# Performance work log

Measured on AMD Instinct MI355X. Metric: run time of the kernel, lower is better.

The kernel has to match this reference:

```python
import jax, jax.numpy as jnp
import numpy as np

HEADS = 16
EMBED = 1024
HEAD_DIM = EMBED // HEADS


def setup_inputs() -> dict:
    key = jax.random.key(0)
    ks = jax.random.split(key, 10)
    B, SQ, SKV = 2, 2048, 2048
    s = 1.0 / np.sqrt(HEAD_DIM)
    sd = 1.0 / np.sqrt(EMBED)
    return {
        "queries": jax.random.normal(ks[0], (B, SQ, EMBED), jnp.float32),
        "values": jax.random.normal(ks[1], (B, SKV, EMBED), jnp.float32),
        "heads": HEADS,
        "Wv": jax.random.normal(ks[2], (HEAD_DIM, HEAD_DIM), jnp.float32) * s,
        "bv": jax.random.normal(ks[3], (HEAD_DIM,), jnp.float32) * 0.02,
        "Wk": jax.random.normal(ks[4], (HEAD_DIM, HEAD_DIM), jnp.float32) * s,
        "bk": jax.random.normal(ks[5], (HEAD_DIM,), jnp.float32) * 0.02,
        "Wq": jax.random.normal(ks[6], (HEAD_DIM, HEAD_DIM), jnp.float32) * s,
        "bq": jax.random.normal(ks[7], (HEAD_DIM,), jnp.float32) * 0.02,
        "Wd": jax.random.normal(ks[8], (EMBED, EMBED), jnp.float32) * sd,
        "bd": jax.random.normal(ks[9], (EMBED,), jnp.float32) * 0.02,
    }


def reference(queries, values, heads, Wv, bv, Wk, bk, Wq, bq, Wd, bd):
    n, sq, e = queries.shape
    skv = values.shape[1]
    d = e // heads
    # reshape to per-head layout [b, s, h, d]
    q_in = queries.reshape(n, sq, heads, d)
    v_in = values.reshape(n, skv, heads, d)
    # shared per-head linear projections (torch Linear: x @ W.T + b)
    v = jnp.einsum("bshd,ed->bshe", v_in, Wv) + bv
    # quirk preserved: keys computed from the ALREADY-PROJECTED values
    k = jnp.einsum("bshd,ed->bshe", v, Wk) + bk
    q = jnp.einsum("bshd,ed->bshe", q_in, Wq) + bq
    # full O(n^2) score matrix [b, h, sq, skv] (as in source)
    scores = jnp.einsum("bqhd,bkhd->bhqk", q, k) / jnp.sqrt(jnp.asarray(d, q.dtype))
    attn = jax.nn.softmax(scores, axis=-1)
    out = jnp.einsum("bhqk,bkhd->bqhd", attn, v).reshape(n, sq, e)
    return out @ Wd.T + bd
```

## Files before the change

### kernel.cpp

```cpp
#include <hip/hip_runtime.h>
#include <hip/hip_bf16.h>
#include <hip/hip_fp16.h>
#include <math.h>

typedef _Float16 f16;
typedef _Float16 f16x8 __attribute__((ext_vector_type(8)));
typedef _Float16 f16x4 __attribute__((ext_vector_type(4)));
typedef _Float16 f16x2 __attribute__((ext_vector_type(2)));
typedef unsigned short u16x8v __attribute__((ext_vector_type(8)));
typedef float f32x4 __attribute__((ext_vector_type(4)));

namespace {
constexpr int B = 2;
constexpr int H = 16;
constexpr int S = 2048;
constexpr int D = 64;
constexpr int E = 1024;
constexpr int LP = 72;
constexpr float QSCALE = 0.125f * 1.4426950408889634f;
}

__global__ void make_wkv(const float* __restrict__ Wk, const float* __restrict__ Wv,
                         const float* __restrict__ bv, const float* __restrict__ bk,
                         float* __restrict__ Wkv, float* __restrict__ bkv) {
  const int g = blockIdx.x * 256 + threadIdx.x;
  const int i = g >> 6, j = g & 63;
  float s = 0.f;
#pragma unroll 16
  for (int d = 0; d < 64; ++d) s = fmaf(Wk[i * 64 + d], Wv[d * 64 + j], s);
  Wkv[g] = s;
  if (g < 64) {
    float bb = bk[g];
#pragma unroll 16
    for (int d = 0; d < 64; ++d) bb = fmaf(Wk[g * 64 + d], bv[d], bb);
    bkv[g] = bb;
  }
}

__global__ __launch_bounds__(256) void cvt_wd(const float* __restrict__ W, f16* __restrict__ out) {
  const int i = blockIdx.x * 256 + threadIdx.x;
  const float4 f = ((const float4*)W)[i];
  f16x4 o;
  o.x = (f16)f.x; o.y = (f16)f.y; o.z = (f16)f.z; o.w = (f16)f.w;
  *(f16x4*)(out + 4 * (size_t)i) = o;
}

__global__ __launch_bounds__(256) void proj_mfma(const float* __restrict__ x,
                                                 const float* __restrict__ W,
                                                 const float* __restrict__ bias,
                                                 f16* __restrict__ out, float scale) {
  const int t = threadIdx.x, lane = t & 63, w = t >> 6;
  const int l15 = lane & 15, quad = lane >> 4;
  const int m0 = (blockIdx.x * 4 + w) * 64;

  f16x8 wf[4][2], af[4][2];
#pragma unroll
  for (int nt = 0; nt < 4; ++nt)
#pragma unroll
    for (int kc = 0; kc < 2; ++kc) {
      const float* g = W + (size_t)(nt * 16 + l15) * 64 + kc * 32 + quad * 8;
      const float4 a = *(const float4*)g, b2 = *(const float4*)(g + 4);
      f16x8 v;
      v[0]=(f16)a.x; v[1]=(f16)a.y; v[2]=(f16)a.z; v[3]=(f16)a.w;
      v[4]=(f16)b2.x; v[5]=(f16)b2.y; v[6]=(f16)b2.z; v[7]=(f16)b2.w;
      wf[nt][kc] = v;
    }
#pragma unroll
  for (int mt = 0; mt < 4; ++mt)
#pragma unroll
    for (int kc = 0; kc < 2; ++kc) {
      const float* g = x + (size_t)(m0 + mt * 16 + l15) * 64 + kc * 32 + quad * 8;
      const float4 a = *(const float4*)g, b2 = *(const float4*)(g + 4);
      f16x8 v;
      v[0]=(f16)a.x; v[1]=(f16)a.y; v[2]=(f16)a.z; v[3]=(f16)a.w;
      v[4]=(f16)b2.x; v[5]=(f16)b2.y; v[6]=(f16)b2.z; v[7]=(f16)b2.w;
      af[mt][kc] = v;
    }

  f32x4 acc[4][4];
#pragma unroll
  for (int mt = 0; mt < 4; ++mt)
#pragma unroll
    for (int nt = 0; nt < 4; ++nt) acc[mt][nt] = (f32x4){0.f, 0.f, 0.f, 0.f};
#pragma unroll
  for (int kc = 0; kc < 2; ++kc)
#pragma unroll
    for (int nt = 0; nt < 4; ++nt)
#pragma unroll
      for (int mt = 0; mt < 4; ++mt)
        acc[mt][nt] = __builtin_amdgcn_mfma_f32_16x16x32_f16(af[mt][kc], wf[nt][kc], acc[mt][nt], 0, 0, 0);

  float bl[4];
#pragma unroll
  for (int nt = 0; nt < 4; ++nt) bl[nt] = bias[nt * 16 + l15];

#pragma unroll
  for (int mt = 0; mt < 4; ++mt)
#pragma unroll
    for (int r = 0; r < 4; ++r) {
      const int g = m0 + mt * 16 + quad * 4 + r;
      const int h = g & 15, bs = g >> 4;
      const int b = bs >> 11, s = bs & 2047;
      f16* o = out + ((size_t)(b * H + h) * S + s) * 64;
#pragma unroll
      for (int nt = 0; nt < 4; ++nt)
        o[nt * 16 + l15] = (f16)((acc[mt][nt][r] + bl[nt]) * scale);
    }
}

__global__ __launch_bounds__(256) void attn_mfma(const f16* __restrict__ qp,
                                                 const f16* __restrict__ kp,
                                                 const f16* __restrict__ vp,
                                                 f16* __restrict__ ao) {
  __shared__ f16 ks[64 * LP];
  __shared__ f16 vt[64 * LP];
  __shared__ f16 ps[4 * 32 * LP];
  const int t = threadIdx.x, lane = t & 63, w = t >> 6;
  const int l15 = lane & 15, quad = lane >> 4;
  const int bh = blockIdx.x;
  const int q0 = blockIdx.y * 128;
  const f16* qbase = qp + ((size_t)bh * S + q0 + w * 32) * D;
  const f16* kbase = kp + (size_t)bh * S * D;
  const f16* vbase = vp + (size_t)bh * S * D;
  f16* pw = ps + w * 32 * LP;

  f16x8 qf[2][2];
#pragma unroll
  for (int mt = 0; mt < 2; ++mt)
#pragma unroll
    for (int kc = 0; kc < 2; ++kc)
      qf[mt][kc] = *(const f16x8*)(qbase + (size_t)(mt * 16 + l15) * D + kc * 32 + quad * 8);

  f16x8 vb4;
#pragma unroll
  for (int j = 0; j < 8; ++j) vb4[j] = (l15 == 0) ? (f16)1.0f : (f16)0.0f;

  f32x4 O[2][5];
#pragma unroll
  for (int mt = 0; mt < 2; ++mt)
#pragma unroll
    for (int nt = 0; nt < 5; ++nt) O[mt][nt] = (f32x4){0.f, 0.f, 0.f, 0.f};

  for (int kt = 0; kt < S / 64; ++kt) {
    __syncthreads();
    {
      const int r = t >> 2, c0 = (t & 3) * 16;
      const f16* g = kbase + ((size_t)kt * 64 + r) * D + c0;
      *(f16x8*)&ks[r * LP + c0] = *(const f16x8*)g;
      *(f16x8*)&ks[r * LP + c0 + 8] = *(const f16x8*)(g + 8);
    }
    {
      const int d0 = (t >> 5) * 8, pc0 = (t & 31) * 2;
      const int kva = (pc0 & 3) * 16 + (pc0 >> 2);
      const u16x8v a = *(const u16x8v*)(vbase + ((size_t)kt * 64 + kva) * D + d0);
      const u16x8v b2 = *(const u16x8v*)(vbase + ((size_t)kt * 64 + kva + 16) * D + d0);
#pragma unroll
      for (int j = 0; j < 8; ++j) {
        const unsigned pk = (unsigned)a[j] | ((unsigned)b2[j] << 16);
        *(unsigned*)&vt[(d0 + j) * LP + pc0] = pk;
      }
    }
    __syncthreads();

    f32x4 sc[2][4];
#pragma unroll
    for (int mt = 0; mt < 2; ++mt)
#pragma unroll
      for (int nt = 0; nt < 4; ++nt) sc[mt][nt] = (f32x4){0.f, 0.f, 0.f, 0.f};
#pragma unroll
    for (int kc = 0; kc < 2; ++kc)
#pragma unroll
      for (int nt = 0; nt < 4; ++nt) {
        const f16x8 bf = *(const f16x8*)&ks[(nt * 16 + l15) * LP + kc * 32 + quad * 8];
#pragma unroll
        for (int mt = 0; mt < 2; ++mt)
          sc[mt][nt] = __builtin_amdgcn_mfma_f32_16x16x32_f16(qf[mt][kc], bf, sc[mt][nt], 0, 0, 0);
      }

#pragma unroll
    for (int mt = 0; mt < 2; ++mt)
#pragma unroll
      for (int r = 0; r < 4; ++r) {
        const float p0 = __builtin_amdgcn_exp2f(sc[mt][0][r]);
        const float p1 = __builtin_amdgcn_exp2f(sc[mt][1][r]);
        const float p2 = __builtin_amdgcn_exp2f(sc[mt][2][r]);
        const float p3 = __builtin_amdgcn_exp2f(sc[mt][3][r]);
        union { f16x4 v4; f16x2 h[2]; } u;
        u.h[0] = __builtin_bit_cast(f16x2, __builtin_amdgcn_cvt_pkrtz(p0, p1));
        u.h[1] = __builtin_bit_cast(f16x2, __builtin_amdgcn_cvt_pkrtz(p2, p3));
        *(f16x4*)&pw[(mt * 16 + quad * 4 + r) * LP + l15 * 4] = u.v4;
      }
    __asm__ volatile("s_waitcnt lgkmcnt(0)" ::: "memory");

    f16x8 pa[2][2];
#pragma unroll
    for (int mt = 0; mt < 2; ++mt)
#pragma unroll
      for (int kc = 0; kc < 2; ++kc)
        pa[mt][kc] = *(const f16x8*)&pw[(mt * 16 + l15) * LP + kc * 32 + quad * 8];
#pragma unroll
    for (int kc = 0; kc < 2; ++kc) {
#pragma unroll
      for (int nt = 0; nt < 4; ++nt) {
        const f16x8 vbf = *(const f16x8*)&vt[(nt * 16 + l15) * LP + kc * 32 + quad * 8];
#pragma unroll
        for (int mt = 0; mt < 2; ++mt)
          O[mt][nt] = __builtin_amdgcn_mfma_f32_16x16x32_f16(pa[mt][kc], vbf, O[mt][nt], 0, 0, 0);
      }
#pragma unroll
      for (int mt = 0; mt < 2; ++mt)
        O[mt][4] = __builtin_amdgcn_mfma_f32_16x16x32_f16(pa[mt][kc], vb4, O[mt][4], 0, 0, 0);
    }
  }

  const int b = bh >> 4, h = bh & 15;
#pragma unroll
  for (int mt = 0; mt < 2; ++mt)
#pragma unroll
    for (int r = 0; r < 4; ++r) {
      const float l = __shfl(O[mt][4][r], quad << 4, 64);
      const float inv = 1.f / l;
      const int row = q0 + w * 32 + mt * 16 + quad * 4 + r;
      f16* o = ao + ((size_t)b * S + row) * E + h * D;
#pragma unroll
      for (int nt = 0; nt < 4; ++nt)
        o[nt * 16 + l15] = (f16)(O[mt][nt][r] * inv);
    }
}

__global__ __launch_bounds__(256) void dense_mfma(const f16* __restrict__ A,
                                                  const f16* __restrict__ Wd16,
                                                  const float* __restrict__ bd,
                                                  float* __restrict__ out) {
  __shared__ f16 as[128 * LP];
  __shared__ f16 bs[128 * LP];
  const int t = threadIdx.x;
  const int lane = t & 63;
  const int w = t >> 6;
  const int l15 = lane & 15;
  const int quad = lane >> 4;
  const int m0 = blockIdx.x * 128;
  const int n0 = blockIdx.y * 128;
  const int wm = (w >> 1) * 64, wn = (w & 1) * 64;

  f32x4 acc[4][4];
#pragma unroll
  for (int mt = 0; mt < 4; ++mt)
#pragma unroll
    for (int nt = 0; nt < 4; ++nt) acc[mt][nt] = (f32x4){0.f, 0.f, 0.f, 0.f};

  for (int kt = 0; kt < E / 64; ++kt) {
    __syncthreads();
    {
      const int r = t >> 1, c0 = (t & 1) * 32;
      const f16* ga = A + (size_t)(m0 + r) * E + kt * 64 + c0;
      const f16* gb = Wd16 + (size_t)(n0 + r) * E + kt * 64 + c0;
#pragma unroll
      for (int c = 0; c < 4; ++c) {
        *(f16x8*)&as[r * LP + c0 + 8 * c] = *(const f16x8*)(ga + 8 * c);
        *(f16x8*)&bs[r * LP + c0 + 8 * c] = *(const f16x8*)(gb + 8 * c);
      }
    }
    __syncthreads();
    f16x8 af[4][2];
#pragma unroll
    for (int mt = 0; mt < 4; ++mt)
#pragma unroll
      for (int kc = 0; kc < 2; ++kc)
        af[mt][kc] = *(const f16x8*)&as[(wm + mt * 16 + l15) * LP + kc * 32 + quad * 8];
#pragma unroll
    for (int kc = 0; kc < 2; ++kc)
#pragma unroll
      for (int nt = 0; nt < 4; ++nt) {
        const f16x8 bf = *(const f16x8*)&bs[(wn + nt * 16 + l15) * LP + kc * 32 + quad * 8];
#pragma unroll
        for (int mt = 0; mt < 4; ++mt)
          acc[mt][nt] = __builtin_amdgcn_mfma_f32_16x16x32_f16(af[mt][kc], bf, acc[mt][nt], 0, 0, 0);
      }
  }
#pragma unroll
  for (int nt = 0; nt < 4; ++nt) {
    const int col = n0 + wn + nt * 16 + l15;
    const float bdv = bd[col];
#pragma unroll
    for (int mt = 0; mt < 4; ++mt)
#pragma unroll
      for (int r = 0; r < 4; ++r)
        out[(size_t)(m0 + wm + mt * 16 + quad * 4 + r) * E + col] = acc[mt][nt][r] + bdv;
  }
}

extern "C" void kernel_launch(void* const* d_in, const int* in_sizes, int n_in,
                              void* d_out, int out_size, void* d_ws, size_t ws_size,
                              hipStream_t stream) {
  const float* queries = (const float*)d_in[0];
  const float* values  = (const float*)d_in[1];
  const float* Wv = (const float*)d_in[3];
  const float* bv = (const float*)d_in[4];
  const float* Wk = (const float*)d_in[5];
  const float* bk = (const float*)d_in[6];
  const float* Wq = (const float*)d_in[7];
  const float* bq = (const float*)d_in[8];
  const float* Wd = (const float*)d_in[9];
  const float* bd = (const float*)d_in[10];
  float* out = (float*)d_out;

  char* ws = (char*)d_ws;
  f16* qp    = (f16*)(ws);
  f16* kp    = (f16*)(ws + 8u * 1024 * 1024);
  f16* vp    = (f16*)(ws + 16u * 1024 * 1024);
  f16* ao    = (f16*)(ws + 24u * 1024 * 1024);
  f16* wd16  = (f16*)(ws + 32u * 1024 * 1024);
  float* wkv = (float*)(ws + 34u * 1024 * 1024);
  float* bkv = (float*)(ws + 34u * 1024 * 1024 + 16384);
  (void)ws_size; (void)in_sizes; (void)n_in; (void)out_size;

  make_wkv<<<16, 256, 0, stream>>>(Wk, Wv, bv, bk, wkv, bkv);
  cvt_wd<<<E * E / 1024, 256, 0, stream>>>(Wd, wd16);
  proj_mfma<<<256, 256, 0, stream>>>(queries, Wq, bq, qp, QSCALE);
  proj_mfma<<<256, 256, 0, stream>>>(values, Wv, bv, vp, 1.0f);
  proj_mfma<<<256, 256, 0, stream>>>(values, wkv, bkv, kp, 1.0f);
  attn_mfma<<<dim3(B * H, S / 128), 256, 0, stream>>>(qp, kp, vp, ao);
  dense_mfma<<<dim3(B * S / 128, E / 128), 256, 0, stream>>>(ao, wd16, bd, out);
}
```

Baseline: 198.6 us.

## Fuse V/K projections, pre-transpose V, load attention and dense operands from global

```diff
diff --git a/kernel.cpp b/kernel.cpp
--- a/kernel.cpp
+++ b/kernel.cpp
@@ -108,12 +108,116 @@
     }
 }
 
-__global__ __launch_bounds__(256) void attn_mfma(const f16* __restrict__ qp,
-                                                 const f16* __restrict__ kp,
-                                                 const f16* __restrict__ vp,
-                                                 f16* __restrict__ ao) {
-  __shared__ f16 ks[64 * LP];
-  __shared__ f16 vt[64 * LP];
+__global__ __launch_bounds__(256) void proj_vk_mfma(const float* __restrict__ x,
+                                                    const float* __restrict__ Wv,
+                                                    const float* __restrict__ bv,
+                                                    const float* __restrict__ Wkv,
+                                                    const float* __restrict__ bkv,
+                                                    f16* __restrict__ vout,
+                                                    f16* __restrict__ kout) {
+  const int t = threadIdx.x, lane = t & 63, w = t >> 6;
+  const int l15 = lane & 15, quad = lane >> 4;
+  const int m0 = (blockIdx.x * 4 + w) * 32;
+
+  f16x8 wfv[4][2], wfk[4][2], af[2][2];
+#pragma unroll
+  for (int nt = 0; nt < 4; ++nt)
+#pragma unroll
+    for (int kc = 0; kc < 2; ++kc) {
+      const size_t off = (size_t)(nt * 16 + l15) * 64 + kc * 32 + quad * 8;
+      {
+        const float4 a = *(const float4*)(Wv + off), b2 = *(const float4*)(Wv + off + 4);
+        f16x8 v;
+        v[0]=(f16)a.x; v[1]=(f16)a.y; v[2]=(f16)a.z; v[3]=(f16)a.w;
+        v[4]=(f16)b2.x; v[5]=(f16)b2.y; v[6]=(f16)b2.z; v[7]=(f16)b2.w;
+        wfv[nt][kc] = v;
+      }
+      {
+        const float4 a = *(const float4*)(Wkv + off), b2 = *(const float4*)(Wkv + off + 4);
+        f16x8 v;
+        v[0]=(f16)a.x; v[1]=(f16)a.y; v[2]=(f16)a.z; v[3]=(f16)a.w;
+        v[4]=(f16)b2.x; v[5]=(f16)b2.y; v[6]=(f16)b2.z; v[7]=(f16)b2.w;
+        wfk[nt][kc] = v;
+      }
+    }
+#pragma unroll
+  for (int mt = 0; mt < 2; ++mt)
+#pragma unroll
+    for (int kc = 0; kc < 2; ++kc) {
+      const float* g = x + (size_t)(m0 + mt * 16 + l15) * 64 + kc * 32 + quad * 8;
+      const float4 a = *(const float4*)g, b2 = *(const float4*)(g + 4);
+      f16x8 v;
+      v[0]=(f16)a.x; v[1]=(f16)a.y; v[2]=(f16)a.z; v[3]=(f16)a.w;
+      v[4]=(f16)b2.x; v[5]=(f16)b2.y; v[6]=(f16)b2.z; v[7]=(f16)b2.w;
+      af[mt][kc] = v;
+    }
+
+  f32x4 accv[2][4], acck[2][4];
+#pragma unroll
+  for (int mt = 0; mt < 2; ++mt)
+#pragma unroll
+    for (int nt = 0; nt < 4; ++nt) {
+      accv[mt][nt] = (f32x4){0.f, 0.f, 0.f, 0.f};
+      acck[mt][nt] = (f32x4){0.f, 0.f, 0.f, 0.f};
+    }
+#pragma unroll
+  for (int kc = 0; kc < 2; ++kc)
+#pragma unroll
+    for (int nt = 0; nt < 4; ++nt)
+#pragma unroll
+      for (int mt = 0; mt < 2; ++mt) {
+        accv[mt][nt] = __builtin_amdgcn_mfma_f32_16x16x32_f16(af[mt][kc], wfv[nt][kc], accv[mt][nt], 0, 0, 0);
+        acck[mt][nt] = __builtin_amdgcn_mfma_f32_16x16x32_f16(af[mt][kc], wfk[nt][kc], acck[mt][nt], 0, 0, 0);
+      }
+
+  float blv[4], blk[4];
+#pragma unroll
+  for (int nt = 0; nt < 4; ++nt) { blv[nt] = bv[nt * 16 + l15]; blk[nt] = bkv[nt * 16 + l15]; }
+
+#pragma unroll
+  for (int mt = 0; mt < 2; ++mt)
+#pragma unroll
+    for (int r = 0; r < 4; ++r) {
+      const int g = m0 + mt * 16 + quad * 4 + r;
+      const int h = g & 15, bs = g >> 4;
+      const int b = bs >> 11, s = bs & 2047;
+      const size_t o = ((size_t)(b * H + h) * S + s) * 64;
+#pragma unroll
+      for (int nt = 0; nt < 4; ++nt) {
+        vout[o + nt * 16 + l15] = (f16)(accv[mt][nt][r] + blv[nt]);
+        kout[o + nt * 16 + l15] = (f16)(acck[mt][nt][r] + blk[nt]);
+      }
+    }
+}
+
+__global__ __launch_bounds__(256) void transpose_v(const f16* __restrict__ vp,
+                                                   f16* __restrict__ vtg) {
+  __shared__ f16 lvt[64 * LP];
+  const int t = threadIdx.x;
+  const int bh = blockIdx.x, kt = blockIdx.y;
+  const f16* vb = vp + ((size_t)bh * S + kt * 64) * D;
+  {
+    const int d0 = (t >> 5) * 8, pc0 = (t & 31) * 2;
+    const int kva = (pc0 & 3) * 16 + (pc0 >> 2);
+    const u16x8v a = *(const u16x8v*)(vb + (size_t)kva * D + d0);
+    const u16x8v b2 = *(const u16x8v*)(vb + (size_t)(kva + 16) * D + d0);
+#pragma unroll
+    for (int j = 0; j < 8; ++j) {
+      const unsigned pk = (unsigned)a[j] | ((unsigned)b2[j] << 16);
+      *(unsigned*)&lvt[(d0 + j) * LP + pc0] = pk;
+    }
+  }
+  __syncthreads();
+  const int d = t >> 2, pc = (t & 3) * 16;
+  f16* o = vtg + ((size_t)bh * D + d) * S + kt * 64 + pc;
+  *(f16x8*)o = *(const f16x8*)&lvt[d * LP + pc];
+  *(f16x8*)(o + 8) = *(const f16x8*)&lvt[d * LP + pc + 8];
+}
+
+__global__ __launch_bounds__(256, 2) void attn_mfma(const f16* __restrict__ qp,
+                                                    const f16* __restrict__ kp,
+                                                    const f16* __restrict__ vtg,
+                                                    f16* __restrict__ ao) {
   __shared__ f16 ps[4 * 32 * LP];
   const int t = threadIdx.x, lane = t & 63, w = t >> 6;
   const int l15 = lane & 15, quad = lane >> 4;
@@ -121,7 +225,7 @@
   const int q0 = blockIdx.y * 128;
   const f16* qbase = qp + ((size_t)bh * S + q0 + w * 32) * D;
   const f16* kbase = kp + (size_t)bh * S * D;
-  const f16* vbase = vp + (size_t)bh * S * D;
+  const f16* vbase = vtg + (size_t)bh * D * S;
   f16* pw = ps + w * 32 * LP;
 
   f16x8 qf[2][2];
@@ -141,26 +245,16 @@
 #pragma unroll
     for (int nt = 0; nt < 5; ++nt) O[mt][nt] = (f32x4){0.f, 0.f, 0.f, 0.f};
 
+  f16x8 kf[2][2][4];
+#pragma unroll
+  for (int kc = 0; kc < 2; ++kc)
+#pragma unroll
+    for (int nt = 0; nt < 4; ++nt)
+      kf[0][kc][nt] = *(const f16x8*)(kbase + (size_t)(nt * 16 + l15) * D + kc * 32 + quad * 8);
+
+#pragma unroll 2
   for (int kt = 0; kt < S / 64; ++kt) {
-    __syncthreads();
-    {
-      const int r = t >> 2, c0 = (t & 3) * 16;
-      const f16* g = kbase + ((size_t)kt * 64 + r) * D + c0;
-      *(f16x8*)&ks[r * LP + c0] = *(const f16x8*)g;
-      *(f16x8*)&ks[r * LP + c0 + 8] = *(const f16x8*)(g + 8);
-    }
-    {
-      const int d0 = (t >> 5) * 8, pc0 = (t & 31) * 2;
-      const int kva = (pc0 & 3) * 16 + (pc0 >> 2);
-      const u16x8v a = *(const u16x8v*)(vbase + ((size_t)kt * 64 + kva) * D + d0);
-      const u16x8v b2 = *(const u16x8v*)(vbase + ((size_t)kt * 64 + kva + 16) * D + d0);
-#pragma unroll
-      for (int j = 0; j < 8; ++j) {
-        const unsigned pk = (unsigned)a[j] | ((unsigned)b2[j] << 16);
-        *(unsigned*)&vt[(d0 + j) * LP + pc0] = pk;
-      }
-    }
-    __syncthreads();
+    const int cur = kt & 1, nxt = cur ^ 1;
 
     f32x4 sc[2][4];
 #pragma unroll
@@ -170,12 +264,24 @@
 #pragma unroll
     for (int kc = 0; kc < 2; ++kc)
 #pragma unroll
-      for (int nt = 0; nt < 4; ++nt) {
-        const f16x8 bf = *(const f16x8*)&ks[(nt * 16 + l15) * LP + kc * 32 + quad * 8];
+      for (int nt = 0; nt < 4; ++nt)
 #pragma unroll
         for (int mt = 0; mt < 2; ++mt)
-          sc[mt][nt] = __builtin_amdgcn_mfma_f32_16x16x32_f16(qf[mt][kc], bf, sc[mt][nt], 0, 0, 0);
-      }
+          sc[mt][nt] = __builtin_amdgcn_mfma_f32_16x16x32_f16(qf[mt][kc], kf[cur][kc][nt], sc[mt][nt], 0, 0, 0);
+
+    const int ktn = (kt + 1) & (S / 64 - 1);
+#pragma unroll
+    for (int kc = 0; kc < 2; ++kc)
+#pragma unroll
+      for (int nt = 0; nt < 4; ++nt)
+        kf[nxt][kc][nt] = *(const f16x8*)(kbase + ((size_t)ktn * 64 + nt * 16 + l15) * D + kc * 32 + quad * 8);
+
+    f16x8 vf[2][4];
+#pragma unroll
+    for (int kc = 0; kc < 2; ++kc)
+#pragma unroll
+      for (int nt = 0; nt < 4; ++nt)
+        vf[kc][nt] = *(const f16x8*)(vbase + (size_t)(nt * 16 + l15) * S + kt * 64 + kc * 32 + quad * 8);
 
 #pragma unroll
     for (int mt = 0; mt < 2; ++mt)
@@ -198,15 +304,14 @@
 #pragma unroll
       for (int kc = 0; kc < 2; ++kc)
         pa[mt][kc] = *(const f16x8*)&pw[(mt * 16 + l15) * LP + kc * 32 + quad * 8];
-#pragma unroll
-    for (int kc = 0; kc < 2; ++kc) {
-#pragma unroll
-      for (int nt = 0; nt < 4; ++nt) {
-        const f16x8 vbf = *(const f16x8*)&vt[(nt * 16 + l15) * LP + kc * 32 + quad * 8];
+
+#pragma unroll
+    for (int kc = 0; kc < 2; ++kc) {
+#pragma unroll
+      for (int nt = 0; nt < 4; ++nt)
 #pragma unroll
         for (int mt = 0; mt < 2; ++mt)
-          O[mt][nt] = __builtin_amdgcn_mfma_f32_16x16x32_f16(pa[mt][kc], vbf, O[mt][nt], 0, 0, 0);
-      }
+          O[mt][nt] = __builtin_amdgcn_mfma_f32_16x16x32_f16(pa[mt][kc], vf[kc][nt], O[mt][nt], 0, 0, 0);
 #pragma unroll
       for (int mt = 0; mt < 2; ++mt)
         O[mt][4] = __builtin_amdgcn_mfma_f32_16x16x32_f16(pa[mt][kc], vb4, O[mt][4], 0, 0, 0);
@@ -232,15 +337,9 @@
                                                   const f16* __restrict__ Wd16,
                                                   const float* __restrict__ bd,
                                                   float* __restrict__ out) {
-  __shared__ f16 as[128 * LP];
-  __shared__ f16 bs[128 * LP];
-  const int t = threadIdx.x;
-  const int lane = t & 63;
-  const int w = t >> 6;
-  const int l15 = lane & 15;
-  const int quad = lane >> 4;
-  const int m0 = blockIdx.x * 128;
-  const int n0 = blockIdx.y * 128;
+  const int t = threadIdx.x, lane = t & 63, w = t >> 6;
+  const int l15 = lane & 15, quad = lane >> 4;
+  const int m0 = blockIdx.x * 128, n0 = blockIdx.y * 128;
   const int wm = (w >> 1) * 64, wn = (w & 1) * 64;
 
   f32x4 acc[4][4];
@@ -249,34 +348,23 @@
 #pragma unroll
     for (int nt = 0; nt < 4; ++nt) acc[mt][nt] = (f32x4){0.f, 0.f, 0.f, 0.f};
 
+#pragma unroll
   for (int kt = 0; kt < E / 64; ++kt) {
-    __syncthreads();
-    {
-      const int r = t >> 1, c0 = (t & 1) * 32;
-      const f16* ga = A + (size_t)(m0 + r) * E + kt * 64 + c0;
-      const f16* gb = Wd16 + (size_t)(n0 + r) * E + kt * 64 + c0;
-#pragma unroll
-      for (int c = 0; c < 4; ++c) {
-        *(f16x8*)&as[r * LP + c0 + 8 * c] = *(const f16x8*)(ga + 8 * c);
-        *(f16x8*)&bs[r * LP + c0 + 8 * c] = *(const f16x8*)(gb + 8 * c);
-      }
-    }
-    __syncthreads();
-    f16x8 af[4][2];
-#pragma unroll
-    for (int mt = 0; mt < 4; ++mt)
-#pragma unroll
-      for (int kc = 0; kc < 2; ++kc)
-        af[mt][kc] = *(const f16x8*)&as[(wm + mt * 16 + l15) * LP + kc * 32 + quad * 8];
-#pragma unroll
-    for (int kc = 0; kc < 2; ++kc)
-#pragma unroll
-      for (int nt = 0; nt < 4; ++nt) {
-        const f16x8 bf = *(const f16x8*)&bs[(wn + nt * 16 + l15) * LP + kc * 32 + quad * 8];
+#pragma unroll
+    for (int kc = 0; kc < 2; ++kc) {
+      f16x8 af[4], bf[4];
+#pragma unroll
+      for (int mt = 0; mt < 4; ++mt)
+        af[mt] = *(const f16x8*)(A + (size_t)(m0 + wm + mt * 16 + l15) * E + kt * 64 + kc * 32 + quad * 8);
+#pragma unroll
+      for (int nt = 0; nt < 4; ++nt)
+        bf[nt] = *(const f16x8*)(Wd16 + (size_t)(n0 + wn + nt * 16 + l15) * E + kt * 64 + kc * 32 + quad * 8);
+#pragma unroll
+      for (int nt = 0; nt < 4; ++nt)
 #pragma unroll
         for (int mt = 0; mt < 4; ++mt)
-          acc[mt][nt] = __builtin_amdgcn_mfma_f32_16x16x32_f16(af[mt][kc], bf, acc[mt][nt], 0, 0, 0);
-      }
+          acc[mt][nt] = __builtin_amdgcn_mfma_f32_16x16x32_f16(af[mt], bf[nt], acc[mt][nt], 0, 0, 0);
+    }
   }
 #pragma unroll
   for (int nt = 0; nt < 4; ++nt) {
@@ -313,13 +401,14 @@
   f16* wd16  = (f16*)(ws + 32u * 1024 * 1024);
   float* wkv = (float*)(ws + 34u * 1024 * 1024);
   float* bkv = (float*)(ws + 34u * 1024 * 1024 + 16384);
+  f16* vtg   = (f16*)(ws + 36u * 1024 * 1024);
   (void)ws_size; (void)in_sizes; (void)n_in; (void)out_size;
 
   make_wkv<<<16, 256, 0, stream>>>(Wk, Wv, bv, bk, wkv, bkv);
   cvt_wd<<<E * E / 1024, 256, 0, stream>>>(Wd, wd16);
   proj_mfma<<<256, 256, 0, stream>>>(queries, Wq, bq, qp, QSCALE);
-  proj_mfma<<<256, 256, 0, stream>>>(values, Wv, bv, vp, 1.0f);
-  proj_mfma<<<256, 256, 0, stream>>>(values, wkv, bkv, kp, 1.0f);
-  attn_mfma<<<dim3(B * H, S / 128), 256, 0, stream>>>(qp, kp, vp, ao);
+  proj_vk_mfma<<<512, 256, 0, stream>>>(values, Wv, bv, wkv, bkv, vp, kp);
+  transpose_v<<<dim3(B * H, S / 64), 256, 0, stream>>>(vp, vtg);
+  attn_mfma<<<dim3(B * H, S / 128), 256, 0, stream>>>(qp, kp, vtg, ao);
   dense_mfma<<<dim3(B * S / 128, E / 128), 256, 0, stream>>>(ao, wd16, bd, out);
 }
```

New measurement: 274.6 us. 1.38x slower.

## Fuse V/K projections, use transposed-V attention, and convert Wd inside the dense GEMM

Applied to the files above, without the earlier changes.

```diff
diff --git a/kernel.cpp b/kernel.cpp
--- a/kernel.cpp
+++ b/kernel.cpp
@@ -7,8 +7,10 @@
 typedef _Float16 f16x8 __attribute__((ext_vector_type(8)));
 typedef _Float16 f16x4 __attribute__((ext_vector_type(4)));
 typedef _Float16 f16x2 __attribute__((ext_vector_type(2)));
-typedef unsigned short u16x8v __attribute__((ext_vector_type(8)));
 typedef float f32x4 __attribute__((ext_vector_type(4)));
+
+#define MFMA16(a, b, c) __builtin_amdgcn_mfma_f32_16x16x16f16((a), (b), (c), 0, 0, 0)
+#define MFMA32(a, b, c) __builtin_amdgcn_mfma_f32_16x16x32_f16((a), (b), (c), 0, 0, 0)
 
 namespace {
 constexpr int B = 2;
@@ -20,40 +22,22 @@
 constexpr float QSCALE = 0.125f * 1.4426950408889634f;
 }
 
-__global__ void make_wkv(const float* __restrict__ Wk, const float* __restrict__ Wv,
-                         const float* __restrict__ bv, const float* __restrict__ bk,
-                         float* __restrict__ Wkv, float* __restrict__ bkv) {
-  const int g = blockIdx.x * 256 + threadIdx.x;
-  const int i = g >> 6, j = g & 63;
-  float s = 0.f;
-#pragma unroll 16
-  for (int d = 0; d < 64; ++d) s = fmaf(Wk[i * 64 + d], Wv[d * 64 + j], s);
-  Wkv[g] = s;
-  if (g < 64) {
-    float bb = bk[g];
-#pragma unroll 16
-    for (int d = 0; d < 64; ++d) bb = fmaf(Wk[g * 64 + d], bv[d], bb);
-    bkv[g] = bb;
-  }
-}
-
-__global__ __launch_bounds__(256) void cvt_wd(const float* __restrict__ W, f16* __restrict__ out) {
-  const int i = blockIdx.x * 256 + threadIdx.x;
-  const float4 f = ((const float4*)W)[i];
-  f16x4 o;
-  o.x = (f16)f.x; o.y = (f16)f.y; o.z = (f16)f.z; o.w = (f16)f.w;
-  *(f16x4*)(out + 4 * (size_t)i) = o;
-}
-
-__global__ __launch_bounds__(256) void proj_mfma(const float* __restrict__ x,
-                                                 const float* __restrict__ W,
-                                                 const float* __restrict__ bias,
-                                                 f16* __restrict__ out, float scale) {
+__device__ __forceinline__ f16x4 cvt4(float a, float b, float c, float d) {
+  union { f16x4 v4; f16x2 h[2]; } u;
+  u.h[0] = __builtin_bit_cast(f16x2, __builtin_amdgcn_cvt_pkrtz(a, b));
+  u.h[1] = __builtin_bit_cast(f16x2, __builtin_amdgcn_cvt_pkrtz(c, d));
+  return u.v4;
+}
+
+__global__ __launch_bounds__(256) void proj_q(const float* __restrict__ x,
+                                              const float* __restrict__ W,
+                                              const float* __restrict__ bias,
+                                              f16* __restrict__ out) {
   const int t = threadIdx.x, lane = t & 63, w = t >> 6;
   const int l15 = lane & 15, quad = lane >> 4;
-  const int m0 = (blockIdx.x * 4 + w) * 64;
-
-  f16x8 wf[4][2], af[4][2];
+  const int m0 = (blockIdx.x * 4 + w) * 32;
+
+  f16x8 wf[4][2], af[2][2];
 #pragma unroll
   for (int nt = 0; nt < 4; ++nt)
 #pragma unroll
@@ -66,7 +50,7 @@
       wf[nt][kc] = v;
     }
 #pragma unroll
-  for (int mt = 0; mt < 4; ++mt)
+  for (int mt = 0; mt < 2; ++mt)
 #pragma unroll
     for (int kc = 0; kc < 2; ++kc) {
       const float* g = x + (size_t)(m0 + mt * 16 + l15) * 64 + kc * 32 + quad * 8;
@@ -77,9 +61,9 @@
       af[mt][kc] = v;
     }
 
-  f32x4 acc[4][4];
-#pragma unroll
-  for (int mt = 0; mt < 4; ++mt)
+  f32x4 acc[2][4];
+#pragma unroll
+  for (int mt = 0; mt < 2; ++mt)
 #pragma unroll
     for (int nt = 0; nt < 4; ++nt) acc[mt][nt] = (f32x4){0.f, 0.f, 0.f, 0.f};
 #pragma unroll
@@ -87,15 +71,15 @@
 #pragma unroll
     for (int nt = 0; nt < 4; ++nt)
 #pragma unroll
-      for (int mt = 0; mt < 4; ++mt)
-        acc[mt][nt] = __builtin_amdgcn_mfma_f32_16x16x32_f16(af[mt][kc], wf[nt][kc], acc[mt][nt], 0, 0, 0);
+      for (int mt = 0; mt < 2; ++mt)
+        acc[mt][nt] = MFMA32(af[mt][kc], wf[nt][kc], acc[mt][nt]);
 
   float bl[4];
 #pragma unroll
   for (int nt = 0; nt < 4; ++nt) bl[nt] = bias[nt * 16 + l15];
 
 #pragma unroll
-  for (int mt = 0; mt < 4; ++mt)
+  for (int mt = 0; mt < 2; ++mt)
 #pragma unroll
     for (int r = 0; r < 4; ++r) {
       const int g = m0 + mt * 16 + quad * 4 + r;
@@ -104,42 +88,132 @@
       f16* o = out + ((size_t)(b * H + h) * S + s) * 64;
 #pragma unroll
       for (int nt = 0; nt < 4; ++nt)
-        o[nt * 16 + l15] = (f16)((acc[mt][nt][r] + bl[nt]) * scale);
-    }
+        o[nt * 16 + l15] = (f16)((acc[mt][nt][r] + bl[nt]) * QSCALE);
+    }
+}
+
+__global__ __launch_bounds__(256) void proj_vk(const float* __restrict__ x,
+                                               const float* __restrict__ Wv,
+                                               const float* __restrict__ bv,
+                                               const float* __restrict__ Wk,
+                                               const float* __restrict__ bk,
+                                               f16* __restrict__ vtg,
+                                               f16* __restrict__ kp) {
+  const int t = threadIdx.x, lane = t & 63, w = t >> 6;
+  const int l15 = lane & 15, quad = lane >> 4;
+  const int bh = blockIdx.x;
+  const int b = bh >> 4, h = bh & 15;
+  const int s0 = blockIdx.y * 128 + w * 32;
+
+  f16x4 xb[2][4];
+#pragma unroll
+  for (int nt = 0; nt < 2; ++nt)
+#pragma unroll
+    for (int kc = 0; kc < 4; ++kc) {
+      const float4 f = *(const float4*)(x + ((size_t)(b * S + s0 + nt * 16 + l15)) * E + h * 64 + kc * 16 + quad * 4);
+      f16x4 v; v[0]=(f16)f.x; v[1]=(f16)f.y; v[2]=(f16)f.z; v[3]=(f16)f.w;
+      xb[nt][kc] = v;
+    }
+
+  f32x4 av[4][2];
+#pragma unroll
+  for (int mt = 0; mt < 4; ++mt)
+#pragma unroll
+    for (int nt = 0; nt < 2; ++nt) av[mt][nt] = (f32x4){0.f, 0.f, 0.f, 0.f};
+#pragma unroll
+  for (int kc = 0; kc < 4; ++kc) {
+    f16x4 wvf[4];
+#pragma unroll
+    for (int mt = 0; mt < 4; ++mt) {
+      const float4 f = *(const float4*)(Wv + (size_t)(mt * 16 + l15) * 64 + kc * 16 + quad * 4);
+      f16x4 v; v[0]=(f16)f.x; v[1]=(f16)f.y; v[2]=(f16)f.z; v[3]=(f16)f.w;
+      wvf[mt] = v;
+    }
+#pragma unroll
+    for (int mt = 0; mt < 4; ++mt)
+#pragma unroll
+      for (int nt = 0; nt < 2; ++nt)
+        av[mt][nt] = MFMA16(wvf[mt], xb[nt][kc], av[mt][nt]);
+  }
+
+  f16x4 vB[4][2];
+#pragma unroll
+  for (int mt = 0; mt < 4; ++mt) {
+    const float4 bb = *(const float4*)(bv + mt * 16 + quad * 4);
+#pragma unroll
+    for (int nt = 0; nt < 2; ++nt) {
+      const float v0 = av[mt][nt][0] + bb.x;
+      const float v1 = av[mt][nt][1] + bb.y;
+      const float v2 = av[mt][nt][2] + bb.z;
+      const float v3 = av[mt][nt][3] + bb.w;
+      const f16x4 pk = cvt4(v0, v1, v2, v3);
+      vB[mt][nt] = pk;
+      const int sc = s0 + nt * 16 + l15;
+      f16* vo = vtg + ((size_t)bh * 64 + mt * 16 + quad * 4) * S + sc;
+      vo[0 * S] = pk[0]; vo[1 * S] = pk[1]; vo[2 * S] = pk[2]; vo[3 * S] = pk[3];
+    }
+  }
+
+  f32x4 ak[4][2];
+#pragma unroll
+  for (int mt = 0; mt < 4; ++mt)
+#pragma unroll
+    for (int nt = 0; nt < 2; ++nt) ak[mt][nt] = (f32x4){0.f, 0.f, 0.f, 0.f};
+#pragma unroll
+  for (int ch = 0; ch < 4; ++ch) {
+    f16x4 wkf[4];
+#pragma unroll
+    for (int mt = 0; mt < 4; ++mt) {
+      const float4 f = *(const float4*)(Wk + (size_t)(mt * 16 + l15) * 64 + ch * 16 + quad * 4);
+      f16x4 v; v[0]=(f16)f.x; v[1]=(f16)f.y; v[2]=(f16)f.z; v[3]=(f16)f.w;
+      wkf[mt] = v;
+    }
+#pragma unroll
+    for (int mt = 0; mt < 4; ++mt)
+#pragma unroll
+      for (int nt = 0; nt < 2; ++nt)
+        ak[mt][nt] = MFMA16(wkf[mt], vB[ch][nt], ak[mt][nt]);
+  }
+#pragma unroll
+  for (int mt = 0; mt < 4; ++mt) {
+    const float4 bb = *(const float4*)(bk + mt * 16 + quad * 4);
+#pragma unroll
+    for (int nt = 0; nt < 2; ++nt) {
+      const int sc = s0 + nt * 16 + l15;
+      const f16x4 pk = cvt4(ak[mt][nt][0] + bb.x, ak[mt][nt][1] + bb.y,
+                            ak[mt][nt][2] + bb.z, ak[mt][nt][3] + bb.w);
+      *(f16x4*)(kp + ((size_t)bh * S + sc) * 64 + mt * 16 + quad * 4) = pk;
+    }
+  }
 }
 
 __global__ __launch_bounds__(256) void attn_mfma(const f16* __restrict__ qp,
                                                  const f16* __restrict__ kp,
-                                                 const f16* __restrict__ vp,
+                                                 const f16* __restrict__ vtg,
                                                  f16* __restrict__ ao) {
   __shared__ f16 ks[64 * LP];
   __shared__ f16 vt[64 * LP];
-  __shared__ f16 ps[4 * 32 * LP];
   const int t = threadIdx.x, lane = t & 63, w = t >> 6;
   const int l15 = lane & 15, quad = lane >> 4;
   const int bh = blockIdx.x;
   const int q0 = blockIdx.y * 128;
   const f16* qbase = qp + ((size_t)bh * S + q0 + w * 32) * D;
   const f16* kbase = kp + (size_t)bh * S * D;
-  const f16* vbase = vp + (size_t)bh * S * D;
-  f16* pw = ps + w * 32 * LP;
-
-  f16x8 qf[2][2];
-#pragma unroll
-  for (int mt = 0; mt < 2; ++mt)
-#pragma unroll
-    for (int kc = 0; kc < 2; ++kc)
-      qf[mt][kc] = *(const f16x8*)(qbase + (size_t)(mt * 16 + l15) * D + kc * 32 + quad * 8);
-
-  f16x8 vb4;
-#pragma unroll
-  for (int j = 0; j < 8; ++j) vb4[j] = (l15 == 0) ? (f16)1.0f : (f16)0.0f;
-
-  f32x4 O[2][5];
-#pragma unroll
-  for (int mt = 0; mt < 2; ++mt)
-#pragma unroll
-    for (int nt = 0; nt < 5; ++nt) O[mt][nt] = (f32x4){0.f, 0.f, 0.f, 0.f};
+  const f16* vbase = vtg + (size_t)bh * 64 * S;
+
+  f16x4 qf[2][4];
+#pragma unroll
+  for (int nt = 0; nt < 2; ++nt)
+#pragma unroll
+    for (int kc = 0; kc < 4; ++kc)
+      qf[nt][kc] = *(const f16x4*)(qbase + (size_t)(nt * 16 + l15) * D + kc * 16 + quad * 4);
+
+  f32x4 Ot[4][2];
+#pragma unroll
+  for (int dt = 0; dt < 4; ++dt)
+#pragma unroll
+    for (int nt = 0; nt < 2; ++nt) Ot[dt][nt] = (f32x4){0.f, 0.f, 0.f, 0.f};
+  float lsum[2] = {0.f, 0.f};
 
   for (int kt = 0; kt < S / 64; ++kt) {
     __syncthreads();
@@ -150,102 +224,93 @@
       *(f16x8*)&ks[r * LP + c0 + 8] = *(const f16x8*)(g + 8);
     }
     {
-      const int d0 = (t >> 5) * 8, pc0 = (t & 31) * 2;
-      const int kva = (pc0 & 3) * 16 + (pc0 >> 2);
-      const u16x8v a = *(const u16x8v*)(vbase + ((size_t)kt * 64 + kva) * D + d0);
-      const u16x8v b2 = *(const u16x8v*)(vbase + ((size_t)kt * 64 + kva + 16) * D + d0);
-#pragma unroll
-      for (int j = 0; j < 8; ++j) {
-        const unsigned pk = (unsigned)a[j] | ((unsigned)b2[j] << 16);
-        *(unsigned*)&vt[(d0 + j) * LP + pc0] = pk;
+      const int r = t >> 2, c0 = (t & 3) * 16;
+      const f16* g = vbase + (size_t)r * S + kt * 64 + c0;
+      *(f16x8*)&vt[r * LP + c0] = *(const f16x8*)g;
+      *(f16x8*)&vt[r * LP + c0 + 8] = *(const f16x8*)(g + 8);
+    }
+    __syncthreads();
+
+    f32x4 sc[4][2];
+#pragma unroll
+    for (int mt = 0; mt < 4; ++mt)
+#pragma unroll
+      for (int nt = 0; nt < 2; ++nt) sc[mt][nt] = (f32x4){0.f, 0.f, 0.f, 0.f};
+#pragma unroll
+    for (int kc = 0; kc < 4; ++kc) {
+      f16x4 ka[4];
+#pragma unroll
+      for (int mt = 0; mt < 4; ++mt)
+        ka[mt] = *(const f16x4*)&ks[(mt * 16 + l15) * LP + kc * 16 + quad * 4];
+#pragma unroll
+      for (int mt = 0; mt < 4; ++mt)
+#pragma unroll
+        for (int nt = 0; nt < 2; ++nt)
+          sc[mt][nt] = MFMA16(ka[mt], qf[nt][kc], sc[mt][nt]);
+    }
+
+    f16x4 pb[4][2];
+#pragma unroll
+    for (int mt = 0; mt < 4; ++mt)
+#pragma unroll
+      for (int nt = 0; nt < 2; ++nt) {
+        const float p0 = __builtin_amdgcn_exp2f(sc[mt][nt][0]);
+        const float p1 = __builtin_amdgcn_exp2f(sc[mt][nt][1]);
+        const float p2 = __builtin_amdgcn_exp2f(sc[mt][nt][2]);
+        const float p3 = __builtin_amdgcn_exp2f(sc[mt][nt][3]);
+        lsum[nt] += (p0 + p1) + (p2 + p3);
+        pb[mt][nt] = cvt4(p0, p1, p2, p3);
       }
-    }
-    __syncthreads();
-
-    f32x4 sc[2][4];
-#pragma unroll
-    for (int mt = 0; mt < 2; ++mt)
-#pragma unroll
-      for (int nt = 0; nt < 4; ++nt) sc[mt][nt] = (f32x4){0.f, 0.f, 0.f, 0.f};
-#pragma unroll
-    for (int kc = 0; kc < 2; ++kc)
-#pragma unroll
-      for (int nt = 0; nt < 4; ++nt) {
-        const f16x8 bf = *(const f16x8*)&ks[(nt * 16 + l15) * LP + kc * 32 + quad * 8];
-#pragma unroll
-        for (int mt = 0; mt < 2; ++mt)
-          sc[mt][nt] = __builtin_amdgcn_mfma_f32_16x16x32_f16(qf[mt][kc], bf, sc[mt][nt], 0, 0, 0);
-      }
-
-#pragma unroll
-    for (int mt = 0; mt < 2; ++mt)
-#pragma unroll
-      for (int r = 0; r < 4; ++r) {
-        const float p0 = __builtin_amdgcn_exp2f(sc[mt][0][r]);
-        const float p1 = __builtin_amdgcn_exp2f(sc[mt][1][r]);
-        const float p2 = __builtin_amdgcn_exp2f(sc[mt][2][r]);
-        const float p3 = __builtin_amdgcn_exp2f(sc[mt][3][r]);
-        union { f16x4 v4; f16x2 h[2]; } u;
-        u.h[0] = __builtin_bit_cast(f16x2, __builtin_amdgcn_cvt_pkrtz(p0, p1));
-        u.h[1] = __builtin_bit_cast(f16x2, __builtin_amdgcn_cvt_pkrtz(p2, p3));
-        *(f16x4*)&pw[(mt * 16 + quad * 4 + r) * LP + l15 * 4] = u.v4;
-      }
-    __asm__ volatile("s_waitcnt lgkmcnt(0)" ::: "memory");
-
-    f16x8 pa[2][2];
-#pragma unroll
-    for (int mt = 0; mt < 2; ++mt)
-#pragma unroll
-      for (int kc = 0; kc < 2; ++kc)
-        pa[mt][kc] = *(const f16x8*)&pw[(mt * 16 + l15) * LP + kc * 32 + quad * 8];
-#pragma unroll
-    for (int kc = 0; kc < 2; ++kc) {
-#pragma unroll
-      for (int nt = 0; nt < 4; ++nt) {
-        const f16x8 vbf = *(const f16x8*)&vt[(nt * 16 + l15) * LP + kc * 32 + quad * 8];
-#pragma unroll
-        for (int mt = 0; mt < 2; ++mt)
-          O[mt][nt] = __builtin_amdgcn_mfma_f32_16x16x32_f16(pa[mt][kc], vbf, O[mt][nt], 0, 0, 0);
-      }
-#pragma unroll
-      for (int mt = 0; mt < 2; ++mt)
-        O[mt][4] = __builtin_amdgcn_mfma_f32_16x16x32_f16(pa[mt][kc], vb4, O[mt][4], 0, 0, 0);
-    }
+
+#pragma unroll
+    for (int mt = 0; mt < 4; ++mt) {
+      f16x4 va[4];
+#pragma unroll
+      for (int dt = 0; dt < 4; ++dt)
+        va[dt] = *(const f16x4*)&vt[(dt * 16 + l15) * LP + mt * 16 + quad * 4];
+#pragma unroll
+      for (int dt = 0; dt < 4; ++dt)
+#pragma unroll
+        for (int nt = 0; nt < 2; ++nt)
+          Ot[dt][nt] = MFMA16(va[dt], pb[mt][nt], Ot[dt][nt]);
+    }
+  }
+
+#pragma unroll
+  for (int nt = 0; nt < 2; ++nt) {
+    lsum[nt] += __shfl_xor(lsum[nt], 16, 64);
+    lsum[nt] += __shfl_xor(lsum[nt], 32, 64);
   }
 
   const int b = bh >> 4, h = bh & 15;
 #pragma unroll
-  for (int mt = 0; mt < 2; ++mt)
-#pragma unroll
-    for (int r = 0; r < 4; ++r) {
-      const float l = __shfl(O[mt][4][r], quad << 4, 64);
-      const float inv = 1.f / l;
-      const int row = q0 + w * 32 + mt * 16 + quad * 4 + r;
-      f16* o = ao + ((size_t)b * S + row) * E + h * D;
-#pragma unroll
-      for (int nt = 0; nt < 4; ++nt)
-        o[nt * 16 + l15] = (f16)(O[mt][nt][r] * inv);
-    }
+  for (int nt = 0; nt < 2; ++nt) {
+    const float inv = 1.f / lsum[nt];
+    const int q = q0 + w * 32 + nt * 16 + l15;
+    f16* o = ao + ((size_t)b * S + q) * E + h * 64;
+#pragma unroll
+    for (int dt = 0; dt < 4; ++dt) {
+      const f16x4 pk = cvt4(Ot[dt][nt][0] * inv, Ot[dt][nt][1] * inv,
+                            Ot[dt][nt][2] * inv, Ot[dt][nt][3] * inv);
+      *(f16x4*)(o + dt * 16 + quad * 4) = pk;
+    }
+  }
 }
 
 __global__ __launch_bounds__(256) void dense_mfma(const f16* __restrict__ A,
-                                                  const f16* __restrict__ Wd16,
+                                                  const float* __restrict__ Wd,
                                                   const float* __restrict__ bd,
                                                   float* __restrict__ out) {
   __shared__ f16 as[128 * LP];
-  __shared__ f16 bs[128 * LP];
-  const int t = threadIdx.x;
-  const int lane = t & 63;
-  const int w = t >> 6;
-  const int l15 = lane & 15;
-  const int quad = lane >> 4;
-  const int m0 = blockIdx.x * 128;
-  const int n0 = blockIdx.y * 128;
-  const int wm = (w >> 1) * 64, wn = (w & 1) * 64;
-
-  f32x4 acc[4][4];
-#pragma unroll
-  for (int mt = 0; mt < 4; ++mt)
+  __shared__ f16 bs[64 * LP];
+  const int t = threadIdx.x, lane = t & 63, w = t >> 6;
+  const int l15 = lane & 15, quad = lane >> 4;
+  const int m0 = blockIdx.x * 128, n0 = blockIdx.y * 64;
+  const int wm = w * 32;
+
+  f32x4 acc[2][4];
+#pragma unroll
+  for (int mt = 0; mt < 2; ++mt)
 #pragma unroll
     for (int nt = 0; nt < 4; ++nt) acc[mt][nt] = (f32x4){0.f, 0.f, 0.f, 0.f};
 
@@ -254,17 +319,26 @@
     {
       const int r = t >> 1, c0 = (t & 1) * 32;
       const f16* ga = A + (size_t)(m0 + r) * E + kt * 64 + c0;
-      const f16* gb = Wd16 + (size_t)(n0 + r) * E + kt * 64 + c0;
-#pragma unroll
-      for (int c = 0; c < 4; ++c) {
+#pragma unroll
+      for (int c = 0; c < 4; ++c)
         *(f16x8*)&as[r * LP + c0 + 8 * c] = *(const f16x8*)(ga + 8 * c);
-        *(f16x8*)&bs[r * LP + c0 + 8 * c] = *(const f16x8*)(gb + 8 * c);
+    }
+    {
+      const int r = t >> 2, c0 = (t & 3) * 16;
+      const float* gb = Wd + (size_t)(n0 + r) * E + kt * 64 + c0;
+#pragma unroll
+      for (int c = 0; c < 2; ++c) {
+        const float4 a = *(const float4*)(gb + 8 * c), b2 = *(const float4*)(gb + 8 * c + 4);
+        f16x8 v;
+        v[0]=(f16)a.x; v[1]=(f16)a.y; v[2]=(f16)a.z; v[3]=(f16)a.w;
+        v[4]=(f16)b2.x; v[5]=(f16)b2.y; v[6]=(f16)b2.z; v[7]=(f16)b2.w;
+        *(f16x8*)&bs[r * LP + c0 + 8 * c] = v;
       }
     }
     __syncthreads();
-    f16x8 af[4][2];
-#pragma unroll
-    for (int mt = 0; mt < 4; ++mt)
+    f16x8 af[2][2];
+#pragma unroll
+    for (int mt = 0; mt < 2; ++mt)
 #pragma unroll
       for (int kc = 0; kc < 2; ++kc)
         af[mt][kc] = *(const f16x8*)&as[(wm + mt * 16 + l15) * LP + kc * 32 + quad * 8];
@@ -272,18 +346,18 @@
     for (int kc = 0; kc < 2; ++kc)
 #pragma unroll
       for (int nt = 0; nt < 4; ++nt) {
-        const f16x8 bf = *(const f16x8*)&bs[(wn + nt * 16 + l15) * LP + kc * 32 + quad * 8];
-#pragma unroll
-        for (int mt = 0; mt < 4; ++mt)
-          acc[mt][nt] = __builtin_amdgcn_mfma_f32_16x16x32_f16(af[mt][kc], bf, acc[mt][nt], 0, 0, 0);
+        const f16x8 bf = *(const f16x8*)&bs[(nt * 16 + l15) * LP + kc * 32 + quad * 8];
+#pragma unroll
+        for (int mt = 0; mt < 2; ++mt)
+          acc[mt][nt] = MFMA32(af[mt][kc], bf, acc[mt][nt]);
       }
   }
 #pragma unroll
   for (int nt = 0; nt < 4; ++nt) {
-    const int col = n0 + wn + nt * 16 + l15;
+    const int col = n0 + nt * 16 + l15;
     const float bdv = bd[col];
 #pragma unroll
-    for (int mt = 0; mt < 4; ++mt)
+    for (int mt = 0; mt < 2; ++mt)
 #pragma unroll
       for (int r = 0; r < 4; ++r)
         out[(size_t)(m0 + wm + mt * 16 + quad * 4 + r) * E + col] = acc[mt][nt][r] + bdv;
@@ -306,20 +380,14 @@
   float* out = (float*)d_out;
 
   char* ws = (char*)d_ws;
-  f16* qp    = (f16*)(ws);
-  f16* kp    = (f16*)(ws + 8u * 1024 * 1024);
-  f16* vp    = (f16*)(ws + 16u * 1024 * 1024);
-  f16* ao    = (f16*)(ws + 24u * 1024 * 1024);
-  f16* wd16  = (f16*)(ws + 32u * 1024 * 1024);
-  float* wkv = (float*)(ws + 34u * 1024 * 1024);
-  float* bkv = (float*)(ws + 34u * 1024 * 1024 + 16384);
+  f16* qp  = (f16*)(ws);
+  f16* kp  = (f16*)(ws + 8u * 1024 * 1024);
+  f16* vtg = (f16*)(ws + 16u * 1024 * 1024);
+  f16* ao  = (f16*)(ws + 24u * 1024 * 1024);
   (void)ws_size; (void)in_sizes; (void)n_in; (void)out_size;
 
-  make_wkv<<<16, 256, 0, stream>>>(Wk, Wv, bv, bk, wkv, bkv);
-  cvt_wd<<<E * E / 1024, 256, 0, stream>>>(Wd, wd16);
-  proj_mfma<<<256, 256, 0, stream>>>(queries, Wq, bq, qp, QSCALE);
-  proj_mfma<<<256, 256, 0, stream>>>(values, Wv, bv, vp, 1.0f);
-  proj_mfma<<<256, 256, 0, stream>>>(values, wkv, bkv, kp, 1.0f);
-  attn_mfma<<<dim3(B * H, S / 128), 256, 0, stream>>>(qp, kp, vp, ao);
-  dense_mfma<<<dim3(B * S / 128, E / 128), 256, 0, stream>>>(ao, wd16, bd, out);
-}
+  proj_q<<<512, 256, 0, stream>>>(queries, Wq, bq, qp);
+  proj_vk<<<dim3(B * H, S / 128), 256, 0, stream>>>(values, Wv, bv, Wk, bk, vtg, kp);
+  attn_mfma<<<dim3(B * H, S / 128), 256, 0, stream>>>(qp, kp, vtg, ao);
+  dense_mfma<<<dim3(B * S / 128, E / 64), 256, 0, stream>>>(ao, Wd, bd, out);
+}
```

Measured after the change: 201.2 us. About the same (+1.3%).
